# Kernel tuning notes

Measured on AMD Instinct MI355X. Metric: run time of the kernel, lower is better.

Reference implementation:

```python
import jax, jax.numpy as jnp
import numpy as np

E = 200      # embsize
R = 480      # num relations
T = 8        # cur_ts (history length)
N = 40000    # num entities
B = 1024     # batch of triples
NEG_INF = -1.0e9


def _lin(x, W, b):
    # torch nn.Linear convention: y = x @ W.T + b
    return x @ W.T + b


def _gru_cell(x, h, wih, whh, bih, bhh):
    # torch GRUCell: gates packed as [r, z, n]
    gi = x @ wih.T + bih
    gh = h @ whh.T + bhh
    i_r, i_z, i_n = jnp.split(gi, 3, axis=1)
    h_r, h_z, h_n = jnp.split(gh, 3, axis=1)
    r = jax.nn.sigmoid(i_r + h_r)
    z = jax.nn.sigmoid(i_z + h_z)
    n = jnp.tanh(i_n + r * h_n)
    return (1.0 - z) * n + z * h


def setup_inputs() -> dict:
    key = jax.random.key(0)
    ks = jax.random.split(key, 24)
    s = 0.05
    pre_emb = jax.random.normal(ks[0], (N, E), dtype=jnp.float32)
    r_emb = jax.random.normal(ks[1], (R, E), dtype=jnp.float32)
    partial_embeding = jax.random.randint(ks[2], (B, T * R), 0, 2).astype(jnp.float32)
    sub = jax.random.randint(ks[3], (B,), 0, N)
    rel = jax.random.randint(ks[4], (B,), 0, R)
    obj = jax.random.randint(ks[5], (B,), 0, N)
    all_triples = jnp.stack([sub, rel, obj], axis=1).astype(jnp.int64)
    params = {
        'W1': jax.random.normal(ks[6], (2 * E, E)) * s, 'b1': jnp.zeros((2 * E,)),
        'W2': jax.random.normal(ks[7], (E, 2 * E)) * s, 'b2': jnp.zeros((E,)),
        'Wa': jax.random.normal(ks[8], (E, E)) * s, 'ba': jnp.zeros((E,)),
        'Wh1': jax.random.normal(ks[9], (E, E)) * s, 'bh1': jnp.zeros((E,)),
        'Wh2': jax.random.normal(ks[10], (E, E)) * s, 'bh2': jnp.zeros((E,)),
        'Wal': jax.random.normal(ks[11], (E, E)) * s, 'bal': jnp.zeros((E,)),
        'gru_wih': jax.random.normal(ks[12], (3 * E, E)) * s,
        'gru_whh': jax.random.normal(ks[13], (3 * E, E)) * s,
        'gru_bih': jnp.zeros((3 * E,)),
        'gru_bhh': jnp.zeros((3 * E,)),
    }
    params = {k: v.astype(jnp.float32) for k, v in params.items()}
    out = {'pre_emb': pre_emb, 'r_emb': r_emb, 'partial_embeding': partial_embeding,
           'all_triples': all_triples, 'cur_ts': T, 'num_rel': R}
    out.update(params)
    return out


def reference(pre_emb, r_emb, partial_embeding, all_triples, cur_ts, num_rel,
              W1, b1, W2, b2, Wa, ba, Wh1, bh1, Wh2, bh2, Wal, bal,
              gru_wih, gru_whh, gru_bih, gru_bhh):
    mapped_rel = _lin(_lin(r_emb, W1, b1), W2, b2)          # [R, E]
    q_rel = mapped_rel[all_triples[:, 1]]                    # [B, E]
    b = partial_embeding.shape[0]

    # loop-invariant attention base: linear_attn(q_rel) @ mapped_rel^T -> [B, R]
    base = _lin(q_rel, Wa, ba) @ mapped_rel.T

    # [B, cur_ts*R] -> [cur_ts, B, R] for scan over timesteps
    pe = partial_embeding.reshape(b, cur_ts, num_rel).transpose(1, 0, 2)

    def step(h, cur):
        attn = cur * base
        attn = jnp.where(attn == 0, jnp.float32(NEG_INF), attn)
        a = jax.nn.softmax(attn, axis=1)
        x = a @ mapped_rel                                   # [B, E]
        h = _gru_cell(x, h, gru_wih, gru_whh, gru_bih, gru_bhh)
        return h, None

    h0 = jnp.zeros((b, mapped_rel.shape[1]), dtype=pre_emb.dtype)
    gru_hidden, _ = jax.lax.scan(step, h0, pe)

    predicted_hist = 0.1 * _lin(_lin(q_rel, Wh1, bh1), Wh2, bh2) + q_rel
    match_loss = jnp.mean((predicted_hist - gru_hidden) ** 2)

    # forward_forth (distmult scoring)
    gru_hidden2 = _gru_cell(q_rel, predicted_hist, gru_wih, gru_whh, gru_bih, gru_bhh)
    sub_emb = pre_emb[all_triples[:, 0]]
    score_logits = (_lin(sub_emb, Wal, bal) * gru_hidden2) @ _lin(pre_emb, Wal, bal).T  # [B, N]
    score = jax.nn.sigmoid(score_logits)

    labels = jnp.zeros_like(score_logits).at[jnp.arange(b), all_triples[:, 2]].set(1.0)
    # stable BCE(sigmoid(s), y)
    path_loss = -jnp.mean(labels * jax.nn.log_sigmoid(score_logits)
                          + (1.0 - labels) * jax.nn.log_sigmoid(-score_logits))
    return (match_loss, path_loss, score)
```

## Files before the change

### kernel.cpp

```cpp
#include <hip/hip_runtime.h>
#include <hip/hip_bf16.h>
#include <math.h>

#define EE 200
#define RR 480
#define TT 8
#define NN 40000
#define BB 1024
#define KP 224
#define GP 672
#define GPR 704
#define LDS_STRIDE 232

typedef __attribute__((ext_vector_type(8))) short short8v;
typedef __attribute__((ext_vector_type(4))) float f32x4;

__device__ inline unsigned short f2bf(float x) {
    unsigned int u = __float_as_uint(x);
    unsigned int r = ((u >> 16) & 1u) + 0x7fffu;
    return (unsigned short)((u + r) >> 16);
}
__device__ inline float bf2f(unsigned short h) {
    return __uint_as_float(((unsigned int)h) << 16);
}
__device__ inline float sigm(float x) { return 1.0f / (1.0f + __expf(-x)); }
__device__ inline void split_store(unsigned short* hi, unsigned short* lo, size_t i, float v) {
    unsigned short h = f2bf(v);
    hi[i] = h;
    lo[i] = f2bf(v - bf2f(h));
}

struct PrepPtrs {
    unsigned short *W1h, *W1l, *W2h, *W2l, *Wabh, *Wabl, *Wh2h, *Wh2l;
    unsigned short *Walh, *Wall, *WTh, *WTl, *wgh, *wgl, *whg, *whl;
    float *bab, *bihp, *bhhp;
    unsigned short *mapSh, *mapSl, *wgiSh, *wgiSl, *hbufs;
    double* acc;
};

__global__ __launch_bounds__(256) void prep_kernel(
    const float* __restrict__ W1, const float* __restrict__ W2,
    const float* __restrict__ Wa, const float* __restrict__ Wh1,
    const float* __restrict__ Wh2, const float* __restrict__ Wal,
    const float* __restrict__ bal, const float* __restrict__ wih,
    const float* __restrict__ whh, const float* __restrict__ ba,
    const float* __restrict__ bh1, const float* __restrict__ bih,
    const float* __restrict__ bhh, PrepPtrs p)
{
    const int gt = blockIdx.x * 256 + threadIdx.x;
    const int gs = gridDim.x * 256;

    for (int i = gt; i < 448 * 224; i += gs) {
        int r = i / 224, c = i - r * 224;
        split_store(p.W1h, p.W1l, i, (r < 400 && c < 200) ? W1[r * 200 + c] : 0.f);
        float vab = 0.f;
        if (c < 200) {
            if (r < 200) vab = Wa[r * 200 + c];
            else if (r >= 224 && r < 424) vab = Wh1[(r - 224) * 200 + c];
        }
        split_store(p.Wabh, p.Wabl, i, vab);
    }
    for (int i = gt; i < 256 * 416; i += gs) {
        int r = i / 416, c = i - r * 416;
        split_store(p.W2h, p.W2l, i, (r < 200 && c < 400) ? W2[r * 400 + c] : 0.f);
    }
    for (int i = gt; i < 256 * 224; i += gs) {
        int r = i / 224, c = i - r * 224;
        bool in = (r < 200 && c < 200);
        split_store(p.Wh2h, p.Wh2l, i, in ? Wh2[r * 200 + c] : 0.f);
        split_store(p.Walh, p.Wall, i, in ? Wal[r * 200 + c] : 0.f);
        float vt = in ? Wal[c * 200 + r] : ((r == 200 && c < 200) ? bal[c] : 0.f);
        split_store(p.WTh, p.WTl, i, vt);
    }
    for (int i = gt; i < 672 * 224; i += gs) {
        int rr = i / 224, c = i - rr * 224;
        int g = rr / 224, j = rr - g * 224;
        bool in = (j < 200 && c < 200);
        split_store(p.wgh, p.wgl, i, in ? wih[(size_t)(g * 200 + j) * 200 + c] : 0.f);
        split_store(p.whg, p.whl, i, in ? whh[(size_t)(g * 200 + j) * 200 + c] : 0.f);
    }
    for (int i = gt; i < 448; i += gs) {
        float v = 0.f;
        if (i < 200) v = ba[i];
        else if (i >= 224 && i < 424) v = bh1[i - 224];
        p.bab[i] = v;
    }
    for (int i = gt; i < GPR; i += gs) {
        int g = i / 224, j = i - g * 224;
        p.bihp[i] = (g < 3 && j < 200) ? bih[g * 200 + j] : 0.f;
    }
    for (int i = gt; i < GP; i += gs) {
        int g = i / 224, j = i - g * 224;
        p.bhhp[i] = (j < 200) ? bhh[g * 200 + j] : 0.f;
    }
    for (int i = gt; i < 512 * 224; i += gs) { p.mapSh[i] = 0; p.mapSl[i] = 0; }
    for (int i = gt; i < 704 * 480; i += gs) { p.wgiSh[i] = 0; p.wgiSl[i] = 0; }
    for (int i = gt; i < 4 * BB * KP; i += gs) p.hbufs[i] = 0;
    if (gt == 0) { p.acc[0] = 0.0; p.acc[1] = 0.0; }
}

template <int MODE, int OUT, int GATHER, int GATEPAD, int EGATHER>
__global__ __launch_bounds__(256) void mfma_flyA(
    const float* __restrict__ A, int lda, const int* __restrict__ gidx, int gsel,
    const unsigned short* __restrict__ Bhi, const unsigned short* __restrict__ Blo,
    const float* __restrict__ bias,
    float* __restrict__ Cf, unsigned short* __restrict__ Chi, unsigned short* __restrict__ Clo,
    int M, int N, int Ka, int Ks,
    const float* __restrict__ extra, int eld, float alpha, int obf)
{
    const int tid = threadIdx.x;
    const int wave = tid >> 6, lane = tid & 63;
    const int r16 = lane & 15, kq = lane >> 4;
    const int kbase = kq * 8;
    const int bm = blockIdx.y * 64 + wave * 16;
    const int bn = blockIdx.x * 64;

    int arow = bm + r16;
    const bool avalid = arow < M;
    if (GATHER) { if (avalid) arow = gidx[arow * 3 + gsel]; }
    const float* Ap = A + (size_t)arow * lda;

    f32x4 acc[4] = {{0,0,0,0},{0,0,0,0},{0,0,0,0},{0,0,0,0}};
    const int nk = Ks >> 5;

    for (int kk = 0; kk < nk; kk++) {
        const int k0 = kk * 32 + kbase;
        short8v a0, a1;
        #pragma unroll
        for (int e = 0; e < 8; e++) {
            float v = (avalid && (k0 + e) < Ka) ? Ap[k0 + e] : 0.f;
            unsigned short h = f2bf(v);
            a0[e] = (short)h;
            a1[e] = (short)f2bf(v - bf2f(h));
        }
        #pragma unroll
        for (int nf = 0; nf < 4; nf++) {
            const size_t boff = (size_t)(bn + nf * 16 + r16) * Ks + k0;
            short8v b0 = *(const short8v*)(Bhi + boff);
            short8v b1 = *(const short8v*)(Blo + boff);
            acc[nf] = __builtin_amdgcn_mfma_f32_16x16x32_bf16(a0, b1, acc[nf], 0, 0, 0);
            acc[nf] = __builtin_amdgcn_mfma_f32_16x16x32_bf16(a1, b0, acc[nf], 0, 0, 0);
            acc[nf] = __builtin_amdgcn_mfma_f32_16x16x32_bf16(a0, b0, acc[nf], 0, 0, 0);
        }
    }

    #pragma unroll
    for (int r = 0; r < 4; r++) {
        const int orow = bm + kq * 4 + r;
        if (orow >= M) continue;
        #pragma unroll
        for (int nf = 0; nf < 4; nf++) {
            const int col = bn + nf * 16 + r16;
            float v = acc[nf][r];
            if (OUT == 0) {
                if (col < N) {
                    if (bias) v += bias[col];
                    if (MODE == 1) {
                        float ex = EGATHER ? extra[(size_t)gidx[orow * 3 + gsel] * eld + col]
                                           : extra[(size_t)orow * eld + col];
                        v = alpha * v + ex;
                    } else if (MODE == 2) {
                        v = v * extra[(size_t)orow * eld + col];
                    }
                    Cf[(size_t)orow * N + col] = v;
                }
            } else if (OUT == 1) {
                if (col < obf) {
                    float w = 0.f;
                    if (col < N) { w = v; if (bias) w += bias[col]; }
                    Chi[(size_t)orow * obf + col] = f2bf(w);
                }
            } else if (OUT == 2) {
                if (col < N) {
                    int wr = GATEPAD ? (orow / 200) * 224 + orow % 200 : orow;
                    if (bias) v += bias[col];
                    split_store(Chi, Clo, (size_t)wr * obf + col, v);
                }
            } else if (OUT == 3) {
                if (col < N) {
                    if (bias) v += bias[col];
                    Cf[(size_t)orow * N + col] = v;
                    split_store(Chi, Clo, (size_t)orow * obf + col, v);
                }
            }
        }
    }
}

__global__ __launch_bounds__(256) void mfma_linear2_kernel(
    const unsigned short* __restrict__ Ahi,
    const unsigned short* __restrict__ Bhi, const unsigned short* __restrict__ Blo,
    const float* __restrict__ bias, float* __restrict__ C,
    int M, int N, int Ks)
{
    const int tid  = threadIdx.x;
    const int wave = tid >> 6;
    const int lane = tid & 63;
    const int r16   = lane & 15;
    const int khalf = lane >> 4;
    const int kbase = khalf * 8;
    const int bm = blockIdx.y * 64 + wave * 16;
    const int bn = blockIdx.x * 64;

    const unsigned short* ah = Ahi + (size_t)(bm + r16) * Ks + kbase;
    const unsigned short* bh = Bhi + (size_t)(bn + r16) * Ks + kbase;
    const unsigned short* bl = Blo + (size_t)(bn + r16) * Ks + kbase;

    f32x4 acc[4] = {{0,0,0,0},{0,0,0,0},{0,0,0,0},{0,0,0,0}};

    for (int k0 = 0; k0 < Ks; k0 += 32) {
        short8v a0 = *(const short8v*)(ah + k0);
        #pragma unroll
        for (int nf = 0; nf < 4; nf++) {
            short8v b0 = *(const short8v*)(bh + (size_t)nf * 16 * Ks + k0);
            short8v b1 = *(const short8v*)(bl + (size_t)nf * 16 * Ks + k0);
            acc[nf] = __builtin_amdgcn_mfma_f32_16x16x32_bf16(a0, b1, acc[nf], 0, 0, 0);
            acc[nf] = __builtin_amdgcn_mfma_f32_16x16x32_bf16(a0, b0, acc[nf], 0, 0, 0);
        }
    }
    #pragma unroll
    for (int r = 0; r < 4; r++) {
        const int row = bm + khalf * 4 + r;
        #pragma unroll
        for (int nf = 0; nf < 4; nf++) {
            const int col = bn + nf * 16 + r16;
            if (col < N)
                C[(size_t)row * N + col] = acc[nf][r] + (bias ? bias[col] : 0.0f);
        }
    }
}

template <int LAST>
__global__ __launch_bounds__(256) void gru_step_kernel(
    const unsigned short* __restrict__ Whi, const unsigned short* __restrict__ Wlo,
    const float* __restrict__ bhh_pad,
    const float* __restrict__ gi_t,
    const unsigned short* __restrict__ hin_hi, const unsigned short* __restrict__ hin_lo,
    unsigned short* __restrict__ hout_hi, unsigned short* __restrict__ hout_lo,
    float* __restrict__ h_fin)
{
    const int tid = threadIdx.x;
    const int wave = tid >> 6, lane = tid & 63;
    const int r16 = lane & 15, kq = lane >> 4;
    const int jf = blockIdx.x;
    const int brow = (blockIdx.y * 4 + wave) * 16;
    const int j = jf * 16 + r16;

    short8v ahi[7], alo[7];
    const unsigned short* hh = hin_hi + (size_t)(brow + r16) * KP + kq * 8;
    const unsigned short* hl = hin_lo + (size_t)(brow + r16) * KP + kq * 8;
    #pragma unroll
    for (int kk = 0; kk < 7; kk++) {
        ahi[kk] = *(const short8v*)(hh + kk * 32);
        alo[kk] = *(const short8v*)(hl + kk * 32);
    }

    f32x4 ar = {0,0,0,0}, az = {0,0,0,0}, an = {0,0,0,0};
    #pragma unroll
    for (int kk = 0; kk < 7; kk++) {
        const size_t rowr = (size_t)(jf * 16 + r16) * KP + kk * 32 + kq * 8;
        const size_t rowz = rowr + (size_t)224 * KP;
        const size_t rown = rowr + (size_t)448 * KP;
        short8v brh = *(const short8v*)(Whi + rowr);
        short8v brl = *(const short8v*)(Wlo + rowr);
        short8v bzh = *(const short8v*)(Whi + rowz);
        short8v bzl = *(const short8v*)(Wlo + rowz);
        short8v bnh = *(const short8v*)(Whi + rown);
        short8v bnl = *(const short8v*)(Wlo + rown);
        ar = __builtin_amdgcn_mfma_f32_16x16x32_bf16(ahi[kk], brl, ar, 0, 0, 0);
        az = __builtin_amdgcn_mfma_f32_16x16x32_bf16(ahi[kk], bzl, az, 0, 0, 0);
        an = __builtin_amdgcn_mfma_f32_16x16x32_bf16(ahi[kk], bnl, an, 0, 0, 0);
        ar = __builtin_amdgcn_mfma_f32_16x16x32_bf16(alo[kk], brh, ar, 0, 0, 0);
        az = __builtin_amdgcn_mfma_f32_16x16x32_bf16(alo[kk], bzh, az, 0, 0, 0);
        an = __builtin_amdgcn_mfma_f32_16x16x32_bf16(alo[kk], bnh, an, 0, 0, 0);
        ar = __builtin_amdgcn_mfma_f32_16x16x32_bf16(ahi[kk], brh, ar, 0, 0, 0);
        az = __builtin_amdgcn_mfma_f32_16x16x32_bf16(ahi[kk], bzh, az, 0, 0, 0);
        an = __builtin_amdgcn_mfma_f32_16x16x32_bf16(ahi[kk], bnh, an, 0, 0, 0);
    }

    const float br = bhh_pad[j], bz = bhh_pad[224 + j], bn_ = bhh_pad[448 + j];
    #pragma unroll
    for (int q = 0; q < 4; q++) {
        const int row = brow + kq * 4 + q;
        float gir = gi_t[(size_t)row * GP + j];
        float giz = gi_t[(size_t)row * GP + 224 + j];
        float gin = gi_t[(size_t)row * GP + 448 + j];
        float r_ = sigm(gir + ar[q] + br);
        float z_ = sigm(giz + az[q] + bz);
        float n_ = tanhf(gin + r_ * (an[q] + bn_));
        float hold = bf2f(hin_hi[(size_t)row * KP + j]) + bf2f(hin_lo[(size_t)row * KP + j]);
        float hnew = (1.0f - z_) * n_ + z_ * hold;
        if (j < EE) {
            unsigned short nh = f2bf(hnew);
            hout_hi[(size_t)row * KP + j] = nh;
            hout_lo[(size_t)row * KP + j] = f2bf(hnew - bf2f(nh));
            if (LAST) h_fin[(size_t)row * EE + j] = hnew;
        }
    }
}

__global__ __launch_bounds__(256) void gru2_fused_kernel(
    const unsigned short* __restrict__ Wihi, const unsigned short* __restrict__ Wilo,
    const unsigned short* __restrict__ Whhi, const unsigned short* __restrict__ Whlo,
    const float* __restrict__ bih_pad, const float* __restrict__ bhh_pad,
    const int* __restrict__ triples, const float* __restrict__ map,
    const float* __restrict__ hp, const float* __restrict__ hfin,
    float* __restrict__ ghid2, double* __restrict__ accMatch)
{
    __shared__ float red[256];
    const int tid = threadIdx.x;
    const int wave = tid >> 6, lane = tid & 63;
    const int r16 = lane & 15, kq = lane >> 4;
    const int jf = blockIdx.x;
    const int brow = (blockIdx.y * 4 + wave) * 16;
    const int j = jf * 16 + r16;

    f32x4 ir = {0,0,0,0}, iz = {0,0,0,0}, in_ = {0,0,0,0};
    f32x4 hr = {0,0,0,0}, hz = {0,0,0,0}, hn = {0,0,0,0};

    {
        const int xrow = triples[(brow + r16) * 3 + 1];
        const float* xp = map + (size_t)xrow * EE;
        #pragma unroll
        for (int kk = 0; kk < 7; kk++) {
            short8v a0, a1;
            #pragma unroll
            for (int e = 0; e < 8; e++) {
                int k = kk * 32 + kq * 8 + e;
                float v = (k < EE) ? xp[k] : 0.0f;
                unsigned short hhh = f2bf(v);
                a0[e] = (short)hhh;
                a1[e] = (short)f2bf(v - bf2f(hhh));
            }
            const size_t rowr = (size_t)(jf * 16 + r16) * KP + kk * 32 + kq * 8;
            const size_t rowz = rowr + (size_t)224 * KP;
            const size_t rown = rowr + (size_t)448 * KP;
            short8v brh = *(const short8v*)(Wihi + rowr);
            short8v brl = *(const short8v*)(Wilo + rowr);
            short8v bzh = *(const short8v*)(Wihi + rowz);
            short8v bzl = *(const short8v*)(Wilo + rowz);
            short8v bnh = *(const short8v*)(Wihi + rown);
            short8v bnl = *(const short8v*)(Wilo + rown);
            ir = __builtin_amdgcn_mfma_f32_16x16x32_bf16(a0, brl, ir, 0, 0, 0);
            iz = __builtin_amdgcn_mfma_f32_16x16x32_bf16(a0, bzl, iz, 0, 0, 0);
            in_ = __builtin_amdgcn_mfma_f32_16x16x32_bf16(a0, bnl, in_, 0, 0, 0);
            ir = __builtin_amdgcn_mfma_f32_16x16x32_bf16(a1, brh, ir, 0, 0, 0);
            iz = __builtin_amdgcn_mfma_f32_16x16x32_bf16(a1, bzh, iz, 0, 0, 0);
            in_ = __builtin_amdgcn_mfma_f32_16x16x32_bf16(a1, bnh, in_, 0, 0, 0);
            ir = __builtin_amdgcn_mfma_f32_16x16x32_bf16(a0, brh, ir, 0, 0, 0);
            iz = __builtin_amdgcn_mfma_f32_16x16x32_bf16(a0, bzh, iz, 0, 0, 0);
            in_ = __builtin_amdgcn_mfma_f32_16x16x32_bf16(a0, bnh, in_, 0, 0, 0);
        }
    }
    {
        const float* hpp = hp + (size_t)(brow + r16) * EE;
        #pragma unroll
        for (int kk = 0; kk < 7; kk++) {
            short8v a0, a1;
            #pragma unroll
            for (int e = 0; e < 8; e++) {
                int k = kk * 32 + kq * 8 + e;
                float v = (k < EE) ? hpp[k] : 0.0f;
                unsigned short hhh = f2bf(v);
                a0[e] = (short)hhh;
                a1[e] = (short)f2bf(v - bf2f(hhh));
            }
            const size_t rowr = (size_t)(jf * 16 + r16) * KP + kk * 32 + kq * 8;
            const size_t rowz = rowr + (size_t)224 * KP;
            const size_t rown = rowr + (size_t)448 * KP;
            short8v brh = *(const short8v*)(Whhi + rowr);
            short8v brl = *(const short8v*)(Whlo + rowr);
            short8v bzh = *(const short8v*)(Whhi + rowz);
            short8v bzl = *(const short8v*)(Whlo + rowz);
            short8v bnh = *(const short8v*)(Whhi + rown);
            short8v bnl = *(const short8v*)(Whlo + rown);
            hr = __builtin_amdgcn_mfma_f32_16x16x32_bf16(a0, brl, hr, 0, 0, 0);
            hz = __builtin_amdgcn_mfma_f32_16x16x32_bf16(a0, bzl, hz, 0, 0, 0);
            hn = __builtin_amdgcn_mfma_f32_16x16x32_bf16(a0, bnl, hn, 0, 0, 0);
            hr = __builtin_amdgcn_mfma_f32_16x16x32_bf16(a1, brh, hr, 0, 0, 0);
            hz = __builtin_amdgcn_mfma_f32_16x16x32_bf16(a1, bzh, hz, 0, 0, 0);
            hn = __builtin_amdgcn_mfma_f32_16x16x32_bf16(a1, bnh, hn, 0, 0, 0);
            hr = __builtin_amdgcn_mfma_f32_16x16x32_bf16(a0, brh, hr, 0, 0, 0);
            hz = __builtin_amdgcn_mfma_f32_16x16x32_bf16(a0, bzh, hz, 0, 0, 0);
            hn = __builtin_amdgcn_mfma_f32_16x16x32_bf16(a0, bnh, hn, 0, 0, 0);
        }
    }

    float psum = 0.0f;
    if (j < EE) {
        const float bir = bih_pad[j], biz = bih_pad[224 + j], bin = bih_pad[448 + j];
        const float bhr = bhh_pad[j], bhz = bhh_pad[224 + j], bhn = bhh_pad[448 + j];
        #pragma unroll
        for (int q = 0; q < 4; q++) {
            const int row = brow + kq * 4 + q;
            float r_ = sigm(ir[q] + bir + hr[q] + bhr);
            float z_ = sigm(iz[q] + biz + hz[q] + bhz);
            float n_ = tanhf(in_[q] + bin + r_ * (hn[q] + bhn));
            float hold = hp[(size_t)row * EE + j];
            ghid2[(size_t)row * EE + j] = (1.0f - z_) * n_ + z_ * hold;
            float d = hold - hfin[(size_t)row * EE + j];
            psum += d * d;
        }
    }
    red[tid] = psum;
    __syncthreads();
    for (int s = 128; s > 0; s >>= 1) {
        if (tid < s) red[tid] += red[tid + s];
        __syncthreads();
    }
    if (tid == 0) atomicAdd(accMatch, (double)red[0]);
}

__global__ __launch_bounds__(512) void score_mfma2_kernel(
    const unsigned short* __restrict__ Ubf,
    const float* __restrict__ pre_emb,
    const int* __restrict__ triples,
    float* __restrict__ outScore,
    double* __restrict__ accPath)
{
    __shared__ unsigned short Bs[64 * LDS_STRIDE];
    __shared__ int objs[BB];
    __shared__ float red[512];

    const int tid = threadIdx.x;
    const int bn = blockIdx.x * 64;

    for (int i = tid; i < BB; i += 512) objs[i] = triples[i * 3 + 2];

    for (int idx = tid; idx < 64 * 50; idx += 512) {
        int row = idx / 50;
        int c4 = (idx - row * 50) * 4;
        float4 v = *(const float4*)(pre_emb + (size_t)(bn + row) * EE + c4);
        unsigned short* d = &Bs[row * LDS_STRIDE + c4];
        d[0] = f2bf(v.x); d[1] = f2bf(v.y); d[2] = f2bf(v.z); d[3] = f2bf(v.w);
    }
    for (int idx = tid; idx < 64 * 24; idx += 512) {
        int row = idx / 24;
        int cc = idx - row * 24;
        Bs[row * LDS_STRIDE + 200 + cc] = (cc == 0) ? (unsigned short)0x3F80 : (unsigned short)0;
    }
    __syncthreads();

    const int wave  = tid >> 6;
    const int lane  = tid & 63;
    const int r16   = lane & 15;
    const int khalf = lane >> 4;
    const int kbase = khalf * 8;

    const unsigned short* bs0 = &Bs[( 0 + r16) * LDS_STRIDE + kbase];
    const unsigned short* bs1 = &Bs[(16 + r16) * LDS_STRIDE + kbase];
    const unsigned short* bs2 = &Bs[(32 + r16) * LDS_STRIDE + kbase];
    const unsigned short* bs3 = &Bs[(48 + r16) * LDS_STRIDE + kbase];

    float psum = 0.0f;

    for (int mi = 0; mi < 8; mi++) {
        const int m0 = mi * 128 + wave * 16;
        const unsigned short* Ap = Ubf + (size_t)(m0 + r16) * KP + kbase;
        f32x4 acc0 = {0,0,0,0}, acc1 = {0,0,0,0}, acc2 = {0,0,0,0}, acc3 = {0,0,0,0};
        #pragma unroll
        for (int k0 = 0; k0 < KP; k0 += 32) {
            short8v a  = *(const short8v*)(Ap + k0);
            short8v b0 = *(const short8v*)(bs0 + k0);
            short8v b1 = *(const short8v*)(bs1 + k0);
            short8v b2 = *(const short8v*)(bs2 + k0);
            short8v b3 = *(const short8v*)(bs3 + k0);
            acc0 = __builtin_amdgcn_mfma_f32_16x16x32_bf16(a, b0, acc0, 0, 0, 0);
            acc1 = __builtin_amdgcn_mfma_f32_16x16x32_bf16(a, b1, acc1, 0, 0, 0);
            acc2 = __builtin_amdgcn_mfma_f32_16x16x32_bf16(a, b2, acc2, 0, 0, 0);
            acc3 = __builtin_amdgcn_mfma_f32_16x16x32_bf16(a, b3, acc3, 0, 0, 0);
        }
        #pragma unroll
        for (int r = 0; r < 4; r++) {
            const int grow = m0 + khalf * 4 + r;
            const int objc = objs[grow];
            float xv[4] = { acc0[r], acc1[r], acc2[r], acc3[r] };
            #pragma unroll
            for (int nf = 0; nf < 4; nf++) {
                const int col = bn + nf * 16 + r16;
                float x  = xv[nf];
                float e  = __expf(-fabsf(x));
                float t1 = 1.0f + e;
                float rc = __builtin_amdgcn_rcpf(t1);
                float sig = (x >= 0.0f) ? rc : e * rc;
                float sp = __logf(t1);
                float s  = (col == objc) ? x : -x;
                psum += fminf(s, 0.0f) - sp;
                outScore[(size_t)grow * NN + col] = sig;
            }
        }
    }
    red[tid] = psum;
    __syncthreads();
    for (int s = 256; s > 0; s >>= 1) {
        if (tid < s) red[tid] += red[tid + s];
        __syncthreads();
    }
    if (tid == 0) atomicAdd(accPath, (double)red[0]);
}

__global__ __launch_bounds__(256) void masked_softmax_all_kernel(
    const float* __restrict__ base, const float* __restrict__ part,
    unsigned short* __restrict__ aout_hi)
{
    __shared__ float sv[RR];
    __shared__ float red[256];
    const int blk = blockIdx.x;
    const int b = blk & (BB - 1);
    const int t = blk >> 10;
    const int tid = threadIdx.x;
    const float* brow = base + (size_t)b * RR;
    const float* prow = part + (size_t)b * (TT * RR) + t * RR;

    float lmax = -3.0e38f;
    for (int r = tid; r < RR; r += 256) {
        float v = prow[r] * brow[r];
        if (v == 0.0f) v = -1000000000.0f;
        sv[r] = v;
        lmax = fmaxf(lmax, v);
    }
    red[tid] = lmax;
    __syncthreads();
    for (int s = 128; s > 0; s >>= 1) {
        if (tid < s) red[tid] = fmaxf(red[tid], red[tid + s]);
        __syncthreads();
    }
    float gmax = red[0];
    __syncthreads();

    float lsum = 0.0f;
    for (int r = tid; r < RR; r += 256) {
        float e = __expf(sv[r] - gmax);
        sv[r] = e;
        lsum += e;
    }
    red[tid] = lsum;
    __syncthreads();
    for (int s = 128; s > 0; s >>= 1) {
        if (tid < s) red[tid] += red[tid + s];
        __syncthreads();
    }
    float inv = 1.0f / red[0];
    for (int r = tid; r < RR; r += 256)
        aout_hi[(size_t)blk * RR + r] = f2bf(sv[r] * inv);
}

__global__ void final_kernel(const double* __restrict__ acc, float* __restrict__ out)
{
    if (threadIdx.x == 0) {
        out[0] = (float)(acc[0] / ((double)BB * EE));
        out[1] = (float)(-acc[1] / ((double)BB * NN));
    }
}

extern "C" void kernel_launch(void* const* d_in, const int* in_sizes, int n_in,
                              void* d_out, int out_size, void* d_ws, size_t ws_size,
                              hipStream_t stream) {
    const float* pre_emb = (const float*)d_in[0];
    const float* r_emb   = (const float*)d_in[1];
    const float* part    = (const float*)d_in[2];
    const int*   triples = (const int*)d_in[3];
    const float* W1  = (const float*)d_in[6];
    const float* b1  = (const float*)d_in[7];
    const float* W2  = (const float*)d_in[8];
    const float* b2  = (const float*)d_in[9];
    const float* Wa  = (const float*)d_in[10];
    const float* ba  = (const float*)d_in[11];
    const float* Wh1 = (const float*)d_in[12];
    const float* bh1 = (const float*)d_in[13];
    const float* Wh2 = (const float*)d_in[14];
    const float* bh2 = (const float*)d_in[15];
    const float* Wal = (const float*)d_in[16];
    const float* bal = (const float*)d_in[17];
    const float* wih = (const float*)d_in[18];
    const float* whh = (const float*)d_in[19];
    const float* bih = (const float*)d_in[20];
    const float* bhh = (const float*)d_in[21];

    float* out = (float*)d_out;
    double* acc = (double*)d_ws;
    float* wsf = (float*)d_ws;
    size_t off = 4;
    auto alloc = [&](size_t n) { float* p = wsf + off; off += (n + 3) & ~(size_t)3; return p; };
    auto allocS = [&](size_t n) { return (unsigned short*)alloc((n + 1) / 2); };

    PrepPtrs p;
    p.W1h  = allocS((size_t)448 * 224);
    p.W1l  = allocS((size_t)448 * 224);
    p.W2h  = allocS((size_t)256 * 416);
    p.W2l  = allocS((size_t)256 * 416);
    p.Wabh = allocS((size_t)448 * 224);
    p.Wabl = allocS((size_t)448 * 224);
    p.Wh2h = allocS((size_t)256 * 224);
    p.Wh2l = allocS((size_t)256 * 224);
    p.Walh = allocS((size_t)256 * 224);
    p.Wall = allocS((size_t)256 * 224);
    p.WTh  = allocS((size_t)256 * 224);
    p.WTl  = allocS((size_t)256 * 224);
    p.wgh  = allocS((size_t)GP * KP);
    p.wgl  = allocS((size_t)GP * KP);
    p.whg  = allocS((size_t)GP * KP);
    p.whl  = allocS((size_t)GP * KP);
    p.bab  = alloc(448);
    p.bihp = alloc(GPR);
    p.bhhp = alloc(GP);
    p.mapSh = allocS((size_t)512 * 224);
    p.mapSl = allocS((size_t)512 * 224);
    p.wgiSh = allocS((size_t)GPR * RR);
    p.wgiSl = allocS((size_t)GPR * RR);
    p.hbufs = allocS((size_t)4 * BB * KP);
    p.acc = acc;

    unsigned short* ha_hi = p.hbufs;
    unsigned short* ha_lo = p.hbufs + (size_t)BB * KP;
    unsigned short* hb_hi = p.hbufs + (size_t)2 * BB * KP;
    unsigned short* hb_lo = p.hbufs + (size_t)3 * BB * KP;

    float* h1     = alloc((size_t)RR * 400);
    float* map    = alloc((size_t)RR * EE);
    float* qa_ph1 = alloc((size_t)BB * 448);
    float* basep  = alloc((size_t)BB * RR);
    unsigned short* aw_hi = allocS((size_t)TT * BB * RR);
    float* gi_all = alloc((size_t)TT * BB * GP);
    float* hfin   = alloc((size_t)BB * EE);
    float* pred   = alloc((size_t)BB * EE);
    float* ghid2  = alloc((size_t)BB * EE);
    float* s1h    = alloc((size_t)BB * EE);
    unsigned short* u_bf = allocS((size_t)BB * KP);

    dim3 blk(256);

    prep_kernel<<<1024, blk, 0, stream>>>(
        W1, W2, Wa, Wh1, Wh2, Wal, bal, wih, whh, ba, bh1, bih, bhh, p);

    mfma_flyA<0,0,0,0,0><<<dim3(7, 8), blk, 0, stream>>>(
        r_emb, 200, nullptr, 0, p.W1h, p.W1l, b1, h1, nullptr, nullptr,
        RR, 400, 200, 224, nullptr, 0, 0.f, 0);
    mfma_flyA<0,3,0,0,0><<<dim3(4, 8), blk, 0, stream>>>(
        h1, 400, nullptr, 0, p.W2h, p.W2l, b2, map, p.mapSh, p.mapSl,
        RR, EE, 400, 416, nullptr, 0, 0.f, 224);
    mfma_flyA<0,0,1,0,0><<<dim3(7, 16), blk, 0, stream>>>(
        map, 200, triples, 1, p.Wabh, p.Wabl, p.bab, qa_ph1, nullptr, nullptr,
        BB, 448, 200, 224, nullptr, 0, 0.f, 0);
    mfma_flyA<0,0,0,0,0><<<dim3(8, 16), blk, 0, stream>>>(
        qa_ph1, 448, nullptr, 0, p.mapSh, p.mapSl, nullptr, basep, nullptr, nullptr,
        BB, RR, 200, 224, nullptr, 0, 0.f, 0);
    masked_softmax_all_kernel<<<TT * BB, blk, 0, stream>>>(basep, part, aw_hi);
    mfma_flyA<0,2,0,1,0><<<dim3(8, 10), blk, 0, stream>>>(
        wih, 200, nullptr, 0, p.mapSh, p.mapSl, nullptr, nullptr, p.wgiSh, p.wgiSl,
        600, RR, 200, 224, nullptr, 0, 0.f, RR);
    mfma_linear2_kernel<<<dim3(11, TT * BB / 64), blk, 0, stream>>>(
        aw_hi, p.wgiSh, p.wgiSl, p.bihp, gi_all, TT * BB, GP, RR);

    for (int t = 0; t < TT; t++) {
        const float* gi_t = gi_all + (size_t)t * BB * GP;
        const unsigned short* ih = (t & 1) ? hb_hi : ha_hi;
        const unsigned short* il = (t & 1) ? hb_lo : ha_lo;
        unsigned short* oh = (t & 1) ? ha_hi : hb_hi;
        unsigned short* ol = (t & 1) ? ha_lo : hb_lo;
        if (t == TT - 1)
            gru_step_kernel<1><<<dim3(13, BB / 64), blk, 0, stream>>>(
                p.whg, p.whl, p.bhhp, gi_t, ih, il, oh, ol, hfin);
        else
            gru_step_kernel<0><<<dim3(13, BB / 64), blk, 0, stream>>>(
                p.whg, p.whl, p.bhhp, gi_t, ih, il, oh, ol, nullptr);
    }

    mfma_flyA<1,0,0,0,1><<<dim3(4, 16), blk, 0, stream>>>(
        qa_ph1 + 224, 448, triples, 1, p.Wh2h, p.Wh2l, bh2, pred, nullptr, nullptr,
        BB, EE, 200, 224, map, 200, 0.1f, 0);
    gru2_fused_kernel<<<dim3(13, BB / 64), blk, 0, stream>>>(
        p.wgh, p.wgl, p.whg, p.whl, p.bihp, p.bhhp,
        triples, map, pred, hfin, ghid2, acc + 0);
    mfma_flyA<2,0,1,0,0><<<dim3(4, 16), blk, 0, stream>>>(
        pre_emb, 200, triples, 0, p.Walh, p.Wall, bal, s1h, nullptr, nullptr,
        BB, EE, 200, 224, ghid2, 200, 0.f, 0);
    mfma_flyA<0,1,0,0,0><<<dim3(4, 16), blk, 0, stream>>>(
        s1h, 200, nullptr, 0, p.WTh, p.WTl, nullptr, nullptr, u_bf, nullptr,
        BB, KP, 200, 224, nullptr, 0, 0.f, KP);
    score_mfma2_kernel<<<NN / 64, dim3(512), 0, stream>>>(u_bf, pre_emb, triples, out + 2, acc + 1);
    final_kernel<<<1, 64, 0, stream>>>(acc, out);
}
```

Before: 442.1 us.

## Fuse GRU scan into one persistent kernel, drop lo-split gi GEMM, retile scoring

The eight per-timestep GRU launches become a single kernel. Each block owns 16 batch rows, keeps the hidden state in LDS across all timesteps, and re-splits it into bf16 hi/lo every step, which removes the inter-step launches and the global hidden-state round trips. The gi GEMM now uses only the hi part of the weights, cutting its MFMAs in half at some precision cost. The scoring kernel is retiled to 32 columns per block with 256 threads, giving more blocks with smaller tiles. The fused scan has only 64 blocks, which may leave much of the GPU idle.

```diff
diff --git a/kernel.cpp b/kernel.cpp
--- a/kernel.cpp
+++ b/kernel.cpp
@@ -34,7 +34,7 @@
     unsigned short *W1h, *W1l, *W2h, *W2l, *Wabh, *Wabl, *Wh2h, *Wh2l;
     unsigned short *Walh, *Wall, *WTh, *WTl, *wgh, *wgl, *whg, *whl;
     float *bab, *bihp, *bhhp;
-    unsigned short *mapSh, *mapSl, *wgiSh, *wgiSl, *hbufs;
+    unsigned short *mapSh, *mapSl, *wgiSh, *wgiSl;
     double* acc;
 };
 
@@ -95,7 +95,6 @@
     }
     for (int i = gt; i < 512 * 224; i += gs) { p.mapSh[i] = 0; p.mapSl[i] = 0; }
     for (int i = gt; i < 704 * 480; i += gs) { p.wgiSh[i] = 0; p.wgiSl[i] = 0; }
-    for (int i = gt; i < 4 * BB * KP; i += gs) p.hbufs[i] = 0;
     if (gt == 0) { p.acc[0] = 0.0; p.acc[1] = 0.0; }
 }
 
@@ -187,9 +186,9 @@
     }
 }
 
-__global__ __launch_bounds__(256) void mfma_linear2_kernel(
+__global__ __launch_bounds__(256) void mfma_linear1_kernel(
     const unsigned short* __restrict__ Ahi,
-    const unsigned short* __restrict__ Bhi, const unsigned short* __restrict__ Blo,
+    const unsigned short* __restrict__ Bhi,
     const float* __restrict__ bias, float* __restrict__ C,
     int M, int N, int Ks)
 {
@@ -204,7 +203,6 @@
 
     const unsigned short* ah = Ahi + (size_t)(bm + r16) * Ks + kbase;
     const unsigned short* bh = Bhi + (size_t)(bn + r16) * Ks + kbase;
-    const unsigned short* bl = Blo + (size_t)(bn + r16) * Ks + kbase;
 
     f32x4 acc[4] = {{0,0,0,0},{0,0,0,0},{0,0,0,0},{0,0,0,0}};
 
@@ -213,8 +211,6 @@
         #pragma unroll
         for (int nf = 0; nf < 4; nf++) {
             short8v b0 = *(const short8v*)(bh + (size_t)nf * 16 * Ks + k0);
-            short8v b1 = *(const short8v*)(bl + (size_t)nf * 16 * Ks + k0);
-            acc[nf] = __builtin_amdgcn_mfma_f32_16x16x32_bf16(a0, b1, acc[nf], 0, 0, 0);
             acc[nf] = __builtin_amdgcn_mfma_f32_16x16x32_bf16(a0, b0, acc[nf], 0, 0, 0);
         }
     }
@@ -230,72 +226,91 @@
     }
 }
 
-template <int LAST>
-__global__ __launch_bounds__(256) void gru_step_kernel(
+__global__ __launch_bounds__(832) void scan_all_kernel(
     const unsigned short* __restrict__ Whi, const unsigned short* __restrict__ Wlo,
     const float* __restrict__ bhh_pad,
-    const float* __restrict__ gi_t,
-    const unsigned short* __restrict__ hin_hi, const unsigned short* __restrict__ hin_lo,
-    unsigned short* __restrict__ hout_hi, unsigned short* __restrict__ hout_lo,
+    const float* __restrict__ gi_all,
     float* __restrict__ h_fin)
 {
+    __shared__ float hsm[16][228];
     const int tid = threadIdx.x;
-    const int wave = tid >> 6, lane = tid & 63;
+    const int wave = tid >> 6;
+    const int lane = tid & 63;
     const int r16 = lane & 15, kq = lane >> 4;
-    const int jf = blockIdx.x;
-    const int brow = (blockIdx.y * 4 + wave) * 16;
+    const int brow = blockIdx.x * 16;
+    const int jf = wave;
     const int j = jf * 16 + r16;
 
-    short8v ahi[7], alo[7];
-    const unsigned short* hh = hin_hi + (size_t)(brow + r16) * KP + kq * 8;
-    const unsigned short* hl = hin_lo + (size_t)(brow + r16) * KP + kq * 8;
-    #pragma unroll
-    for (int kk = 0; kk < 7; kk++) {
-        ahi[kk] = *(const short8v*)(hh + kk * 32);
-        alo[kk] = *(const short8v*)(hl + kk * 32);
-    }
-
-    f32x4 ar = {0,0,0,0}, az = {0,0,0,0}, an = {0,0,0,0};
-    #pragma unroll
-    for (int kk = 0; kk < 7; kk++) {
-        const size_t rowr = (size_t)(jf * 16 + r16) * KP + kk * 32 + kq * 8;
-        const size_t rowz = rowr + (size_t)224 * KP;
-        const size_t rown = rowr + (size_t)448 * KP;
-        short8v brh = *(const short8v*)(Whi + rowr);
-        short8v brl = *(const short8v*)(Wlo + rowr);
-        short8v bzh = *(const short8v*)(Whi + rowz);
-        short8v bzl = *(const short8v*)(Wlo + rowz);
-        short8v bnh = *(const short8v*)(Whi + rown);
-        short8v bnl = *(const short8v*)(Wlo + rown);
-        ar = __builtin_amdgcn_mfma_f32_16x16x32_bf16(ahi[kk], brl, ar, 0, 0, 0);
-        az = __builtin_amdgcn_mfma_f32_16x16x32_bf16(ahi[kk], bzl, az, 0, 0, 0);
-        an = __builtin_amdgcn_mfma_f32_16x16x32_bf16(ahi[kk], bnl, an, 0, 0, 0);
-        ar = __builtin_amdgcn_mfma_f32_16x16x32_bf16(alo[kk], brh, ar, 0, 0, 0);
-        az = __builtin_amdgcn_mfma_f32_16x16x32_bf16(alo[kk], bzh, az, 0, 0, 0);
-        an = __builtin_amdgcn_mfma_f32_16x16x32_bf16(alo[kk], bnh, an, 0, 0, 0);
-        ar = __builtin_amdgcn_mfma_f32_16x16x32_bf16(ahi[kk], brh, ar, 0, 0, 0);
-        az = __builtin_amdgcn_mfma_f32_16x16x32_bf16(ahi[kk], bzh, az, 0, 0, 0);
-        an = __builtin_amdgcn_mfma_f32_16x16x32_bf16(ahi[kk], bnh, an, 0, 0, 0);
-    }
+    for (int i = tid; i < 16 * 228; i += 832) ((float*)hsm)[i] = 0.0f;
+    __syncthreads();
 
     const float br = bhh_pad[j], bz = bhh_pad[224 + j], bn_ = bhh_pad[448 + j];
-    #pragma unroll
-    for (int q = 0; q < 4; q++) {
-        const int row = brow + kq * 4 + q;
-        float gir = gi_t[(size_t)row * GP + j];
-        float giz = gi_t[(size_t)row * GP + 224 + j];
-        float gin = gi_t[(size_t)row * GP + 448 + j];
-        float r_ = sigm(gir + ar[q] + br);
-        float z_ = sigm(giz + az[q] + bz);
-        float n_ = tanhf(gin + r_ * (an[q] + bn_));
-        float hold = bf2f(hin_hi[(size_t)row * KP + j]) + bf2f(hin_lo[(size_t)row * KP + j]);
-        float hnew = (1.0f - z_) * n_ + z_ * hold;
+
+    for (int t = 0; t < TT; t++) {
+        short8v ahi[7], alo[7];
+        #pragma unroll
+        for (int kk = 0; kk < 7; kk++) {
+            float v[8];
+            *(float4*)&v[0] = *(const float4*)&hsm[r16][kk * 32 + kq * 8];
+            *(float4*)&v[4] = *(const float4*)&hsm[r16][kk * 32 + kq * 8 + 4];
+            short8v h8, l8;
+            #pragma unroll
+            for (int e = 0; e < 8; e++) {
+                unsigned short hh = f2bf(v[e]);
+                h8[e] = (short)hh;
+                l8[e] = (short)f2bf(v[e] - bf2f(hh));
+            }
+            ahi[kk] = h8; alo[kk] = l8;
+        }
+
+        f32x4 ar = {0,0,0,0}, az = {0,0,0,0}, an = {0,0,0,0};
+        #pragma unroll
+        for (int kk = 0; kk < 7; kk++) {
+            const size_t rowr = (size_t)(jf * 16 + r16) * KP + kk * 32 + kq * 8;
+            const size_t rowz = rowr + (size_t)224 * KP;
+            const size_t rown = rowr + (size_t)448 * KP;
+            short8v brh = *(const short8v*)(Whi + rowr);
+            short8v brl = *(const short8v*)(Wlo + rowr);
+            short8v bzh = *(const short8v*)(Whi + rowz);
+            short8v bzl = *(const short8v*)(Wlo + rowz);
+            short8v bnh = *(const short8v*)(Whi + rown);
+            short8v bnl = *(const short8v*)(Wlo + rown);
+            ar = __builtin_amdgcn_mfma_f32_16x16x32_bf16(ahi[kk], brl, ar, 0, 0, 0);
+            az = __builtin_amdgcn_mfma_f32_16x16x32_bf16(ahi[kk], bzl, az, 0, 0, 0);
+            an = __builtin_amdgcn_mfma_f32_16x16x32_bf16(ahi[kk], bnl, an, 0, 0, 0);
+            ar = __builtin_amdgcn_mfma_f32_16x16x32_bf16(alo[kk], brh, ar, 0, 0, 0);
+            az = __builtin_amdgcn_mfma_f32_16x16x32_bf16(alo[kk], bzh, az, 0, 0, 0);
+            an = __builtin_amdgcn_mfma_f32_16x16x32_bf16(alo[kk], bnh, an, 0, 0, 0);
+            ar = __builtin_amdgcn_mfma_f32_16x16x32_bf16(ahi[kk], brh, ar, 0, 0, 0);
+            az = __builtin_amdgcn_mfma_f32_16x16x32_bf16(ahi[kk], bzh, az, 0, 0, 0);
+            an = __builtin_amdgcn_mfma_f32_16x16x32_bf16(ahi[kk], bnh, an, 0, 0, 0);
+        }
+
+        const float* gi_t = gi_all + ((size_t)t * BB + brow) * GP;
+        float hnew[4];
+        #pragma unroll
+        for (int q = 0; q < 4; q++) {
+            const int row = kq * 4 + q;
+            float gir = gi_t[(size_t)row * GP + j];
+            float giz = gi_t[(size_t)row * GP + 224 + j];
+            float gin = gi_t[(size_t)row * GP + 448 + j];
+            float r_ = sigm(gir + ar[q] + br);
+            float z_ = sigm(giz + az[q] + bz);
+            float n_ = tanhf(gin + r_ * (an[q] + bn_));
+            float hold = hsm[row][j];
+            hnew[q] = (1.0f - z_) * n_ + z_ * hold;
+        }
+        __syncthreads();
         if (j < EE) {
-            unsigned short nh = f2bf(hnew);
-            hout_hi[(size_t)row * KP + j] = nh;
-            hout_lo[(size_t)row * KP + j] = f2bf(hnew - bf2f(nh));
-            if (LAST) h_fin[(size_t)row * EE + j] = hnew;
-        }
+            #pragma unroll
+            for (int q = 0; q < 4; q++) hsm[kq * 4 + q][j] = hnew[q];
+        }
+        __syncthreads();
+    }
+
+    for (int i = tid; i < 16 * EE; i += 832) {
+        int r = i / EE, c = i - r * EE;
+        h_fin[(size_t)(brow + r) * EE + c] = hsm[r][c];
     }
 }
 
@@ -411,30 +426,30 @@
     if (tid == 0) atomicAdd(accMatch, (double)red[0]);
 }
 
-__global__ __launch_bounds__(512) void score_mfma2_kernel(
+__global__ __launch_bounds__(256) void score_mfma2_kernel(
     const unsigned short* __restrict__ Ubf,
     const float* __restrict__ pre_emb,
     const int* __restrict__ triples,
     float* __restrict__ outScore,
     double* __restrict__ accPath)
 {
-    __shared__ unsigned short Bs[64 * LDS_STRIDE];
+    __shared__ unsigned short Bs[32 * LDS_STRIDE];
     __shared__ int objs[BB];
-    __shared__ float red[512];
+    __shared__ float red[256];
 
     const int tid = threadIdx.x;
-    const int bn = blockIdx.x * 64;
-
-    for (int i = tid; i < BB; i += 512) objs[i] = triples[i * 3 + 2];
-
-    for (int idx = tid; idx < 64 * 50; idx += 512) {
+    const int bn = blockIdx.x * 32;
+
+    for (int i = tid; i < BB; i += 256) objs[i] = triples[i * 3 + 2];
+
+    for (int idx = tid; idx < 32 * 50; idx += 256) {
         int row = idx / 50;
         int c4 = (idx - row * 50) * 4;
         float4 v = *(const float4*)(pre_emb + (size_t)(bn + row) * EE + c4);
         unsigned short* d = &Bs[row * LDS_STRIDE + c4];
         d[0] = f2bf(v.x); d[1] = f2bf(v.y); d[2] = f2bf(v.z); d[3] = f2bf(v.w);
     }
-    for (int idx = tid; idx < 64 * 24; idx += 512) {
+    for (int idx = tid; idx < 32 * 24; idx += 256) {
         int row = idx / 24;
         int cc = idx - row * 24;
         Bs[row * LDS_STRIDE + 200 + cc] = (cc == 0) ? (unsigned short)0x3F80 : (unsigned short)0;
@@ -449,34 +464,28 @@
 
     const unsigned short* bs0 = &Bs[( 0 + r16) * LDS_STRIDE + kbase];
     const unsigned short* bs1 = &Bs[(16 + r16) * LDS_STRIDE + kbase];
-    const unsigned short* bs2 = &Bs[(32 + r16) * LDS_STRIDE + kbase];
-    const unsigned short* bs3 = &Bs[(48 + r16) * LDS_STRIDE + kbase];
 
     float psum = 0.0f;
 
-    for (int mi = 0; mi < 8; mi++) {
-        const int m0 = mi * 128 + wave * 16;
+    for (int mi = 0; mi < 16; mi++) {
+        const int m0 = mi * 64 + wave * 16;
         const unsigned short* Ap = Ubf + (size_t)(m0 + r16) * KP + kbase;
-        f32x4 acc0 = {0,0,0,0}, acc1 = {0,0,0,0}, acc2 = {0,0,0,0}, acc3 = {0,0,0,0};
+        f32x4 acc0 = {0,0,0,0}, acc1 = {0,0,0,0};
         #pragma unroll
         for (int k0 = 0; k0 < KP; k0 += 32) {
             short8v a  = *(const short8v*)(Ap + k0);
             short8v b0 = *(const short8v*)(bs0 + k0);
             short8v b1 = *(const short8v*)(bs1 + k0);
-            short8v b2 = *(const short8v*)(bs2 + k0);
-            short8v b3 = *(const short8v*)(bs3 + k0);
             acc0 = __builtin_amdgcn_mfma_f32_16x16x32_bf16(a, b0, acc0, 0, 0, 0);
             acc1 = __builtin_amdgcn_mfma_f32_16x16x32_bf16(a, b1, acc1, 0, 0, 0);
-            acc2 = __builtin_amdgcn_mfma_f32_16x16x32_bf16(a, b2, acc2, 0, 0, 0);
-            acc3 = __builtin_amdgcn_mfma_f32_16x16x32_bf16(a, b3, acc3, 0, 0, 0);
         }
         #pragma unroll
         for (int r = 0; r < 4; r++) {
             const int grow = m0 + khalf * 4 + r;
             const int objc = objs[grow];
-            float xv[4] = { acc0[r], acc1[r], acc2[r], acc3[r] };
+            float xv[2] = { acc0[r], acc1[r] };
             #pragma unroll
-            for (int nf = 0; nf < 4; nf++) {
+            for (int nf = 0; nf < 2; nf++) {
                 const int col = bn + nf * 16 + r16;
                 float x  = xv[nf];
                 float e  = __expf(-fabsf(x));
@@ -492,7 +501,7 @@
     }
     red[tid] = psum;
     __syncthreads();
-    for (int s = 256; s > 0; s >>= 1) {
+    for (int s = 128; s > 0; s >>= 1) {
         if (tid < s) red[tid] += red[tid + s];
         __syncthreads();
     }
@@ -608,13 +617,7 @@
     p.mapSl = allocS((size_t)512 * 224);
     p.wgiSh = allocS((size_t)GPR * RR);
     p.wgiSl = allocS((size_t)GPR * RR);
-    p.hbufs = allocS((size_t)4 * BB * KP);
     p.acc = acc;
-
-    unsigned short* ha_hi = p.hbufs;
-    unsigned short* ha_lo = p.hbufs + (size_t)BB * KP;
-    unsigned short* hb_hi = p.hbufs + (size_t)2 * BB * KP;
-    unsigned short* hb_lo = p.hbufs + (size_t)3 * BB * KP;
 
     float* h1     = alloc((size_t)RR * 400);
     float* map    = alloc((size_t)RR * EE);
@@ -649,22 +652,11 @@
     mfma_flyA<0,2,0,1,0><<<dim3(8, 10), blk, 0, stream>>>(
         wih, 200, nullptr, 0, p.mapSh, p.mapSl, nullptr, nullptr, p.wgiSh, p.wgiSl,
         600, RR, 200, 224, nullptr, 0, 0.f, RR);
-    mfma_linear2_kernel<<<dim3(11, TT * BB / 64), blk, 0, stream>>>(
-        aw_hi, p.wgiSh, p.wgiSl, p.bihp, gi_all, TT * BB, GP, RR);
-
-    for (int t = 0; t < TT; t++) {
-        const float* gi_t = gi_all + (size_t)t * BB * GP;
-        const unsigned short* ih = (t & 1) ? hb_hi : ha_hi;
-        const unsigned short* il = (t & 1) ? hb_lo : ha_lo;
-        unsigned short* oh = (t & 1) ? ha_hi : hb_hi;
-        unsigned short* ol = (t & 1) ? ha_lo : hb_lo;
-        if (t == TT - 1)
-            gru_step_kernel<1><<<dim3(13, BB / 64), blk, 0, stream>>>(
-                p.whg, p.whl, p.bhhp, gi_t, ih, il, oh, ol, hfin);
-        else
-            gru_step_kernel<0><<<dim3(13, BB / 64), blk, 0, stream>>>(
-                p.whg, p.whl, p.bhhp, gi_t, ih, il, oh, ol, nullptr);
-    }
+    mfma_linear1_kernel<<<dim3(11, TT * BB / 64), blk, 0, stream>>>(
+        aw_hi, p.wgiSh, p.bihp, gi_all, TT * BB, GP, RR);
+
+    scan_all_kernel<<<BB / 16, dim3(832), 0, stream>>>(
+        p.whg, p.whl, p.bhhp, gi_all, hfin);
 
     mfma_flyA<1,0,0,0,1><<<dim3(4, 16), blk, 0, stream>>>(
         qa_ph1 + 224, 448, triples, 1, p.Wh2h, p.Wh2l, bh2, pred, nullptr, nullptr,
@@ -678,6 +670,6 @@
     mfma_flyA<0,1,0,0,0><<<dim3(4, 16), blk, 0, stream>>>(
         s1h, 200, nullptr, 0, p.WTh, p.WTl, nullptr, nullptr, u_bf, nullptr,
         BB, KP, 200, 224, nullptr, 0, 0.f, KP);
-    score_mfma2_kernel<<<NN / 64, dim3(512), 0, stream>>>(u_bf, pre_emb, triples, out + 2, acc + 1);
+    score_mfma2_kernel<<<NN / 32, blk, 0, stream>>>(u_bf, pre_emb, triples, out + 2, acc + 1);
     final_kernel<<<1, 64, 0, stream>>>(acc, out);
 }
```

New measurement: 452.2 us. 2.3% more time.
